# Kernel optimization log

Hardware: AMD Instinct MI355X
Metric: run time of the kernel (lower is better)

Reference implementation:

```python
import jax, jax.numpy as jnp
import numpy as np

H_DIM, W_DIM, D_MODEL = 128, 128, 1024
N_HEADS, HEAD_DIM = 16, 64


def setup_inputs() -> dict:
    key = jax.random.key(0)
    ks = jax.random.split(key, 8)
    s = D_MODEL ** -0.5
    return {
        "hidden_state": jax.random.normal(ks[0], (H_DIM, W_DIM, D_MODEL), jnp.float32),
        "attn_mask": jnp.zeros((1, 1, W_DIM, W_DIM), jnp.float32),
        "cos": jax.random.uniform(ks[1], (H_DIM, W_DIM, 1, HEAD_DIM), jnp.float32),
        "sin": jax.random.uniform(ks[2], (H_DIM, W_DIM, 1, HEAD_DIM), jnp.float32),
        "Wq": jax.random.normal(ks[3], (D_MODEL, N_HEADS * HEAD_DIM), jnp.float32) * s,
        "Wk": jax.random.normal(ks[4], (D_MODEL, N_HEADS * HEAD_DIM), jnp.float32) * s,
        "Wv": jax.random.normal(ks[5], (D_MODEL, N_HEADS * HEAD_DIM), jnp.float32) * s,
        "Wo": jax.random.normal(ks[6], (2 * D_MODEL, D_MODEL), jnp.float32) * s,
    }


def _rotate_half(x):
    x1, x2 = jnp.split(x, 2, axis=-1)
    return jnp.concatenate((-x2, x1), axis=-1)


def reference(hidden_state, attn_mask, cos, sin, Wq, Wk, Wv, Wo):
    h, w, d = hidden_state.shape
    Dh = cos.shape[-1]
    nH = d // Dh
    # projections (no bias) + RoPE on q/k
    q = (hidden_state @ Wq).reshape(h, w, nH, Dh)
    k = (hidden_state @ Wk).reshape(h, w, nH, Dh)
    v = (hidden_state @ Wv).reshape(h, w, nH, Dh)
    q = q * cos + _rotate_half(q) * sin
    k = k * cos + _rotate_half(k) * sin
    # NOTE: original divides by sqrt(hidden_size), not sqrt(head_dim)
    scale = jnp.sqrt(jnp.asarray(d, hidden_state.dtype))
    # ---- width attention: (h, w, nH, Dh) -> (h, nH, w, Dh) ----
    qx, kx, vx = (t.transpose(0, 2, 1, 3) for t in (q, k, v))
    sx = jnp.einsum('ahqd,ahkd->ahqk', qx, kx) / scale + attn_mask  # (h, nH, w, w)
    ow = jnp.einsum('ahqk,ahkd->ahqd', jax.nn.softmax(sx, axis=-1), vx)
    w_weights = ow.transpose(0, 2, 1, 3)  # (h, w, nH, Dh)
    # ---- height attention: (h, w, nH, Dh) -> (w, nH, h, Dh) ----
    qy, ky, vy = (t.transpose(1, 2, 0, 3) for t in (q, k, v))
    my = jnp.transpose(attn_mask, (2, 1, 0, 3))
    sy = jnp.einsum('ahqd,ahkd->ahqk', qy, ky) / scale + my  # (w, nH, h, h)
    oh = jnp.einsum('ahqk,ahkd->ahqd', jax.nn.softmax(sy, axis=-1), vy)
    h_weights = oh.transpose(2, 0, 1, 3)  # (h, w, nH, Dh)
    cat = jnp.concatenate([w_weights.reshape(h, w, d), h_weights.reshape(h, w, d)], axis=-1)
    return cat @ Wo
```

## Files before the change

kernel.cpp:

```cpp
#include <hip/hip_runtime.h>

typedef unsigned short u16;
typedef unsigned int   u32;
typedef __bf16 bf16;
typedef bf16  bf16x8 __attribute__((ext_vector_type(8)));
typedef float f32x4  __attribute__((ext_vector_type(4)));

__device__ __forceinline__ u16 bf16u(float f) {
    u32 x = __builtin_bit_cast(u32, f);
    x += 0x7fffu + ((x >> 16) & 1u);
    return (u16)(x >> 16);
}

__device__ __forceinline__ void gl_lds16(const void* g, void* l) {
    __builtin_amdgcn_global_load_lds(
        (const __attribute__((address_space(1))) u32*)g,
        (__attribute__((address_space(3))) u32*)l, 16, 0, 0);
}

__global__ __launch_bounds__(256) void cvt_x_kernel(const float4* __restrict__ in,
                                                    ushort4* __restrict__ out, int n4) {
    int i = blockIdx.x * 256 + threadIdx.x;
    if (i >= n4) return;
    float4 f = in[i];
    ushort4 o;
    o.x = bf16u(f.x); o.y = bf16u(f.y); o.z = bf16u(f.z); o.w = bf16u(f.w);
    out[i] = o;
}

__global__ __launch_bounds__(256) void transp_all(
    const float* __restrict__ Wq, const float* __restrict__ Wk,
    const float* __restrict__ Wv, const float* __restrict__ Wo,
    u16* __restrict__ WqkvT, u16* __restrict__ WoT)
{
    const int z = blockIdx.z;
    const float* W; u16* WT; int rows, cols;
    if (z < 3) {
        if (blockIdx.y >= 32) return;
        W = (z == 0) ? Wq : (z == 1) ? Wk : Wv;
        WT = WqkvT + (size_t)z * 1024 * 1024;
        rows = 1024; cols = 1024;
    } else {
        W = Wo; WT = WoT; rows = 2048; cols = 1024;
    }
    __shared__ float t[32][33];
    int bx = blockIdx.x * 32, by = blockIdx.y * 32;
    int x = threadIdx.x & 31, y = threadIdx.x >> 5;
#pragma unroll
    for (int i = 0; i < 32; i += 8)
        t[y + i][x] = W[(size_t)(by + y + i) * cols + bx + x];
    __syncthreads();
#pragma unroll
    for (int i = 0; i < 32; i += 8)
        WT[(size_t)(bx + y + i) * rows + by + x] = bf16u(t[x][y + i]);
}

#define BAR   __builtin_amdgcn_s_barrier()
#define SB0   __builtin_amdgcn_sched_barrier(0)
#define VM4   asm volatile("s_waitcnt vmcnt(4)" ::: "memory")
#define VM0   asm volatile("s_waitcnt vmcnt(0)" ::: "memory")

__global__ __launch_bounds__(512, 2) void gemm8(
    const u16* __restrict__ A, const u16* __restrict__ BT, void* __restrict__ Cout,
    const float* __restrict__ cosp, const float* __restrict__ sinp,
    int M, int N, int K, int mode)
{
    __shared__ u16 Ld[3][16384];
    const int tid = threadIdx.x;
    const int wid = tid >> 6, lane = tid & 63;
    const int nx = gridDim.x;
    const int nwg = nx * gridDim.y;
    const int orig = blockIdx.y * nx + blockIdx.x;
    const int vid = (orig & 7) * (nwg >> 3) + (orig >> 3);
    const int m0 = (vid / nx) << 8, n0 = (vid % nx) << 8;
    const int wr = wid >> 2, wc = wid & 3;

    const int srow = tid >> 2;
    const int sl = (tid & 3) ^ ((srow >> 1) & 3);
    const u16* aS0 = A + (size_t)(m0 + srow) * K + (sl << 3);
    const u16* aS1 = aS0 + (size_t)128 * K;
    const u16* bS0 = BT + (size_t)(n0 + srow) * K + (sl << 3);
    const u16* bS1 = bS0 + (size_t)128 * K;
    const int wdb = wid << 9;
    const int nt = K >> 5;

#define STAGE(T, B_) do { if ((T) < nt) { size_t _ko = (size_t)(T) << 5; \
        gl_lds16(aS0 + _ko, &Ld[B_][wdb]); \
        gl_lds16(aS1 + _ko, &Ld[B_][4096 + wdb]); \
        gl_lds16(bS0 + _ko, &Ld[B_][8192 + wdb]); \
        gl_lds16(bS1 + _ko, &Ld[B_][12288 + wdb]); } } while (0)

    const int phys = ((lane >> 4) ^ ((lane >> 1) & 3)) << 3;
    const int raw = ((wr << 7) + (lane & 15)) << 5;
    const int rbw = (((wc << 6) + (lane & 15)) << 5) + 8192;

    f32x4 acc[8][4] = {};

    STAGE(0, 0); STAGE(1, 1);
    VM4;
    BAR; SB0;

    int b = 0, bs = 2;
    for (int t = 0; t < nt; ++t) {
        const u16* Lb = &Ld[b][0];
        bf16x8 fa[8], fb[4];
#pragma unroll
        for (int mi = 0; mi < 8; mi++)
            fa[mi] = *(const bf16x8*)&Lb[raw + (mi << 9) + phys];
#pragma unroll
        for (int ni = 0; ni < 4; ni++)
            fb[ni] = *(const bf16x8*)&Lb[rbw + (ni << 9) + phys];
        STAGE(t + 2, bs);
        BAR;
        __builtin_amdgcn_s_setprio(1);
#pragma unroll
        for (int mi = 0; mi < 8; mi++)
#pragma unroll
            for (int ni = 0; ni < 4; ni++)
                acc[mi][ni] = __builtin_amdgcn_mfma_f32_16x16x32_bf16(
                    fa[mi], fb[ni], acc[mi][ni], 0, 0, 0);
        __builtin_amdgcn_s_setprio(0);
        if (t + 2 < nt) { VM4; } else { VM0; }
        BAR; SB0;
        b = (b == 2) ? 0 : b + 1;
        bs = (bs == 2) ? 0 : bs + 1;
    }
#undef STAGE

    const int colbase = n0 + (wc << 6) + (lane & 15);
    if (mode == 2) {
        float* C = (float*)Cout;
#pragma unroll
        for (int mi = 0; mi < 8; mi++)
#pragma unroll
            for (int r = 0; r < 4; r++) {
                int m = m0 + (wr << 7) + (mi << 4) + ((lane >> 4) << 2) + r;
                float* row = C + (size_t)m * N + colbase;
#pragma unroll
                for (int ni = 0; ni < 4; ni++) row[ni << 4] = acc[mi][ni][r];
            }
    } else if (n0 < 2048) {
        u16* C = (u16*)Cout;
#pragma unroll
        for (int mi = 0; mi < 8; mi++)
#pragma unroll
            for (int r = 0; r < 4; r++) {
                int m = m0 + (wr << 7) + (mi << 4) + ((lane >> 4) << 2) + r;
                const float* cb = cosp + ((size_t)m << 6);
                const float* sb = sinp + ((size_t)m << 6);
                u16* row = C + (size_t)m * N + colbase;
#pragma unroll
                for (int ni = 0; ni < 4; ni++) {
                    int d = (ni << 4) + (lane & 15);
                    float c = cb[d], s = sb[d];
                    float v0 = acc[mi][ni][r];
                    float vr = acc[mi][ni ^ 2][r];
                    float o = fmaf(v0, c, (ni < 2 ? -vr : vr) * s);
                    row[ni << 4] = bf16u(o);
                }
            }
    } else {
        u16* C = (u16*)Cout;
#pragma unroll
        for (int mi = 0; mi < 8; mi++)
#pragma unroll
            for (int r = 0; r < 4; r++) {
                int m = m0 + (wr << 7) + (mi << 4) + ((lane >> 4) << 2) + r;
                u16* row = C + (size_t)m * N + colbase;
#pragma unroll
                for (int ni = 0; ni < 4; ni++) row[ni << 4] = bf16u(acc[mi][ni][r]);
            }
    }
}

__global__ __launch_bounds__(256) void axial_attn(
    const u16* __restrict__ qkv, const float* __restrict__ mask,
    u16* __restrict__ cat)
{
    __shared__ u16 Kl[128 * 64];
    __shared__ u16 VT[64 * 128];
    __shared__ u16 Pl[128 * 128];
    const int hmode = blockIdx.x >> 11;
    const int o2 = blockIdx.x & 2047;
    const int b = (o2 & 7) * 256 + (o2 >> 3);
    const int a = b >> 4, hd = b & 15;
    const int tid = threadIdx.x, wid = tid >> 6, lane = tid & 63;
    const int tmul = hmode ? 128 : 1;
    const int tadd = hmode ? a : (a << 7);
    const size_t hoff = (size_t)hd << 6;

#pragma unroll
    for (int c = 0; c < 4; c++) {
        int row = (wid << 5) + (c << 3) + (lane >> 3);
        int sc = (lane & 7) ^ (row & 7);
        gl_lds16(qkv + (size_t)(row * tmul + tadd) * 3072 + 1024 + hoff + (sc << 3),
                 &Kl[((wid << 5) + (c << 3)) << 6]);
    }
#pragma unroll
    for (int i = 0; i < 4; i++) {
        int cid = tid + (i << 8);
        int j = cid >> 3;
        int d0 = (cid & 7) << 3;
        uint4 raw = *(const uint4*)(qkv + (size_t)(j * tmul + tadd) * 3072 + 2048 + hoff + d0);
        const u16* e = (const u16*)&raw;
#pragma unroll
        for (int t = 0; t < 8; t++) {
            int d = d0 + t;
            VT[(d << 7) + (((j >> 3) ^ (d & 15)) << 3) + (j & 7)] = e[t];
        }
    }
    bf16x8 aq[2][2];
#pragma unroll
    for (int qt = 0; qt < 2; qt++)
#pragma unroll
        for (int ks = 0; ks < 2; ks++) {
            int row = (wid << 5) + (qt << 4) + (lane & 15);
            aq[qt][ks] = *(const bf16x8*)(qkv + (size_t)(row * tmul + tadd) * 3072 + hoff
                                          + (ks << 5) + ((lane >> 4) << 3));
        }
    __syncthreads();

    f32x4 S[2][8] = {};
#pragma unroll
    for (int kt = 0; kt < 8; kt++) {
        bf16x8 bk[2];
#pragma unroll
        for (int ks = 0; ks < 2; ks++) {
            int row = (kt << 4) + (lane & 15);
            int ch = ((ks << 2) + (lane >> 4)) ^ (row & 7);
            bk[ks] = *(const bf16x8*)&Kl[(row << 6) + (ch << 3)];
        }
#pragma unroll
        for (int qt = 0; qt < 2; qt++) {
            S[qt][kt] = __builtin_amdgcn_mfma_f32_16x16x32_bf16(aq[qt][0], bk[0], S[qt][kt], 0, 0, 0);
            S[qt][kt] = __builtin_amdgcn_mfma_f32_16x16x32_bf16(aq[qt][1], bk[1], S[qt][kt], 0, 0, 0);
        }
    }

    const float scale = 0.03125f;
#pragma unroll
    for (int qt = 0; qt < 2; qt++) {
#pragma unroll
        for (int r = 0; r < 4; r++) {
            int qrow = (wid << 5) + (qt << 4) + ((lane >> 4) << 2) + r;
            const float* mrow = mask + (hmode ? (a << 7) : (qrow << 7));
            float mx = -1e30f;
#pragma unroll
            for (int kt = 0; kt < 8; kt++) {
                float sv = fmaf(S[qt][kt][r], scale, mrow[(kt << 4) + (lane & 15)]);
                S[qt][kt][r] = sv;
                mx = fmaxf(mx, sv);
            }
            mx = fmaxf(mx, __shfl_xor(mx, 1));
            mx = fmaxf(mx, __shfl_xor(mx, 2));
            mx = fmaxf(mx, __shfl_xor(mx, 4));
            mx = fmaxf(mx, __shfl_xor(mx, 8));
            float sum = 0.f;
#pragma unroll
            for (int kt = 0; kt < 8; kt++) {
                float p = __expf(S[qt][kt][r] - mx);
                S[qt][kt][r] = p;
                sum += p;
            }
            sum += __shfl_xor(sum, 1);
            sum += __shfl_xor(sum, 2);
            sum += __shfl_xor(sum, 4);
            sum += __shfl_xor(sum, 8);
            float rinv = 1.0f / sum;
#pragma unroll
            for (int kt = 0; kt < 8; kt++) {
                int kcol = (kt << 4) + (lane & 15);
                int ch = (kcol >> 3) ^ (qrow & 15);
                Pl[(qrow << 7) + (ch << 3) + (kcol & 7)] = bf16u(S[qt][kt][r] * rinv);
            }
        }
    }
    __syncthreads();

    f32x4 O[4][2] = {};
#pragma unroll
    for (int ks = 0; ks < 4; ks++) {
        bf16x8 av[4], bp[2];
#pragma unroll
        for (int dt = 0; dt < 4; dt++) {
            int drow = (dt << 4) + (lane & 15);
            int ch = ((ks << 2) + (lane >> 4)) ^ (drow & 15);
            av[dt] = *(const bf16x8*)&VT[(drow << 7) + (ch << 3)];
        }
#pragma unroll
        for (int qt = 0; qt < 2; qt++) {
            int qrow = (wid << 5) + (qt << 4) + (lane & 15);
            int ch = ((ks << 2) + (lane >> 4)) ^ (qrow & 15);
            bp[qt] = *(const bf16x8*)&Pl[(qrow << 7) + (ch << 3)];
        }
#pragma unroll
        for (int dt = 0; dt < 4; dt++)
#pragma unroll
            for (int qt = 0; qt < 2; qt++)
                O[dt][qt] = __builtin_amdgcn_mfma_f32_16x16x32_bf16(av[dt], bp[qt], O[dt][qt], 0, 0, 0);
    }

    const int cbase = (hmode ? 1024 : 0) + (hd << 6);
#pragma unroll
    for (int dt = 0; dt < 4; dt++)
#pragma unroll
        for (int qt = 0; qt < 2; qt++) {
            int qrow = (wid << 5) + (qt << 4) + (lane & 15);
            int d0 = (dt << 4) + ((lane >> 4) << 2);
            size_t base = ((size_t)(qrow * tmul + tadd) << 11) + cbase + d0;
            ushort4 pk;
            pk.x = bf16u(O[dt][qt][0]);
            pk.y = bf16u(O[dt][qt][1]);
            pk.z = bf16u(O[dt][qt][2]);
            pk.w = bf16u(O[dt][qt][3]);
            *(ushort4*)(cat + base) = pk;
        }
}

extern "C" void kernel_launch(void* const* d_in, const int* in_sizes, int n_in,
                              void* d_out, int out_size, void* d_ws, size_t ws_size,
                              hipStream_t stream)
{
    (void)in_sizes; (void)n_in; (void)out_size; (void)ws_size;
    const float* hidden = (const float*)d_in[0];
    const float* mask   = (const float*)d_in[1];
    const float* cosp   = (const float*)d_in[2];
    const float* sinp   = (const float*)d_in[3];
    const float* Wq     = (const float*)d_in[4];
    const float* Wk     = (const float*)d_in[5];
    const float* Wv     = (const float*)d_in[6];
    const float* Wo     = (const float*)d_in[7];

    char* ws = (char*)d_ws;
    u16* Xb    = (u16*)(ws);
    u16* WqkvT = (u16*)(ws + 33554432);
    u16* cat   = (u16*)(ws);
    u16* WoT   = (u16*)(ws + 67108864);
    u16* qkvb  = (u16*)(ws + 71303168);

    cvt_x_kernel<<<16384, 256, 0, stream>>>((const float4*)hidden, (ushort4*)Xb, 4194304);
    transp_all<<<dim3(32, 64, 4), 256, 0, stream>>>(Wq, Wk, Wv, Wo, WqkvT, WoT);

    gemm8<<<dim3(12, 64), 512, 0, stream>>>(Xb, WqkvT, qkvb, cosp, sinp, 16384, 3072, 1024, 1);

    axial_attn<<<4096, 256, 0, stream>>>(qkvb, mask, cat);

    gemm8<<<dim3(4, 64), 512, 0, stream>>>(cat, WoT, d_out, nullptr, nullptr, 16384, 1024, 2048, 2);
}
```

Baseline: 316.9 us.

## Replace triple-buffered 256x256 GEMM with simple single-buffer 128x128 tile GEMM

Swaps the 512-thread, 256x256-tile GEMM with a three-stage LDS pipeline for a 256-thread, 128x128-tile kernel that uses a single LDS buffer. Each K-step loads, then synchronizes, then computes. Grids are doubled in both dimensions to cover the outputs. This reduces LDS and register footprint per block and raises block count, but it drops the load/compute overlap and halves data reuse per tile, which likely exposes memory latency.

```diff
diff --git a/kernel.cpp b/kernel.cpp
--- a/kernel.cpp
+++ b/kernel.cpp
@@ -55,86 +55,69 @@
         WT[(size_t)(bx + y + i) * rows + by + x] = bf16u(t[x][y + i]);
 }
 
-#define BAR   __builtin_amdgcn_s_barrier()
-#define SB0   __builtin_amdgcn_sched_barrier(0)
-#define VM4   asm volatile("s_waitcnt vmcnt(4)" ::: "memory")
-#define VM0   asm volatile("s_waitcnt vmcnt(0)" ::: "memory")
-
-__global__ __launch_bounds__(512, 2) void gemm8(
+__global__ __launch_bounds__(256) void gemm97(
     const u16* __restrict__ A, const u16* __restrict__ BT, void* __restrict__ Cout,
     const float* __restrict__ cosp, const float* __restrict__ sinp,
     int M, int N, int K, int mode)
 {
-    __shared__ u16 Ld[3][16384];
+    __shared__ u16 Ld[8192];
     const int tid = threadIdx.x;
     const int wid = tid >> 6, lane = tid & 63;
     const int nx = gridDim.x;
     const int nwg = nx * gridDim.y;
     const int orig = blockIdx.y * nx + blockIdx.x;
     const int vid = (orig & 7) * (nwg >> 3) + (orig >> 3);
-    const int m0 = (vid / nx) << 8, n0 = (vid % nx) << 8;
-    const int wr = wid >> 2, wc = wid & 3;
+    const int m0 = (vid / nx) << 7, n0 = (vid % nx) << 7;
+    const int wr = wid >> 1, wc = wid & 1;
 
     const int srow = tid >> 2;
-    const int sl = (tid & 3) ^ ((srow >> 1) & 3);
-    const u16* aS0 = A + (size_t)(m0 + srow) * K + (sl << 3);
-    const u16* aS1 = aS0 + (size_t)128 * K;
-    const u16* bS0 = BT + (size_t)(n0 + srow) * K + (sl << 3);
-    const u16* bS1 = bS0 + (size_t)128 * K;
+    const int sg = (tid & 3) ^ ((srow >> 1) & 3);
+    const u16* aS = A + (size_t)(m0 + srow) * K + (sg << 3);
+    const u16* bS = BT + (size_t)(n0 + srow) * K + (sg << 3);
+    const size_t h64K = (size_t)64 * K;
     const int wdb = wid << 9;
     const int nt = K >> 5;
 
-#define STAGE(T, B_) do { if ((T) < nt) { size_t _ko = (size_t)(T) << 5; \
-        gl_lds16(aS0 + _ko, &Ld[B_][wdb]); \
-        gl_lds16(aS1 + _ko, &Ld[B_][4096 + wdb]); \
-        gl_lds16(bS0 + _ko, &Ld[B_][8192 + wdb]); \
-        gl_lds16(bS1 + _ko, &Ld[B_][12288 + wdb]); } } while (0)
-
     const int phys = ((lane >> 4) ^ ((lane >> 1) & 3)) << 3;
-    const int raw = ((wr << 7) + (lane & 15)) << 5;
-    const int rbw = (((wc << 6) + (lane & 15)) << 5) + 8192;
-
-    f32x4 acc[8][4] = {};
-
-    STAGE(0, 0); STAGE(1, 1);
-    VM4;
-    BAR; SB0;
-
-    int b = 0, bs = 2;
+    const int raw = ((wr << 6) + (lane & 15)) << 5;
+    const int rbw = (((wc << 6) + (lane & 15)) << 5) + 4096;
+
+    f32x4 acc[4][4] = {};
+
     for (int t = 0; t < nt; ++t) {
-        const u16* Lb = &Ld[b][0];
-        bf16x8 fa[8], fb[4];
-#pragma unroll
-        for (int mi = 0; mi < 8; mi++)
-            fa[mi] = *(const bf16x8*)&Lb[raw + (mi << 9) + phys];
-#pragma unroll
-        for (int ni = 0; ni < 4; ni++)
-            fb[ni] = *(const bf16x8*)&Lb[rbw + (ni << 9) + phys];
-        STAGE(t + 2, bs);
-        BAR;
+        if (t) __syncthreads();
+        const size_t ko = (size_t)t << 5;
+        gl_lds16(aS + ko,        &Ld[wdb]);
+        gl_lds16(aS + ko + h64K, &Ld[2048 + wdb]);
+        gl_lds16(bS + ko,        &Ld[4096 + wdb]);
+        gl_lds16(bS + ko + h64K, &Ld[6144 + wdb]);
+        __syncthreads();
+
+        bf16x8 af[4], bfr[4];
+#pragma unroll
+        for (int i = 0; i < 4; i++)
+            af[i] = *(const bf16x8*)&Ld[raw + (i << 9) + phys];
+#pragma unroll
+        for (int i = 0; i < 4; i++)
+            bfr[i] = *(const bf16x8*)&Ld[rbw + (i << 9) + phys];
         __builtin_amdgcn_s_setprio(1);
 #pragma unroll
-        for (int mi = 0; mi < 8; mi++)
+        for (int mi = 0; mi < 4; mi++)
 #pragma unroll
             for (int ni = 0; ni < 4; ni++)
                 acc[mi][ni] = __builtin_amdgcn_mfma_f32_16x16x32_bf16(
-                    fa[mi], fb[ni], acc[mi][ni], 0, 0, 0);
+                    af[mi], bfr[ni], acc[mi][ni], 0, 0, 0);
         __builtin_amdgcn_s_setprio(0);
-        if (t + 2 < nt) { VM4; } else { VM0; }
-        BAR; SB0;
-        b = (b == 2) ? 0 : b + 1;
-        bs = (bs == 2) ? 0 : bs + 1;
-    }
-#undef STAGE
+    }
 
     const int colbase = n0 + (wc << 6) + (lane & 15);
     if (mode == 2) {
         float* C = (float*)Cout;
 #pragma unroll
-        for (int mi = 0; mi < 8; mi++)
+        for (int mi = 0; mi < 4; mi++)
 #pragma unroll
             for (int r = 0; r < 4; r++) {
-                int m = m0 + (wr << 7) + (mi << 4) + ((lane >> 4) << 2) + r;
+                int m = m0 + (wr << 6) + (mi << 4) + ((lane >> 4) << 2) + r;
                 float* row = C + (size_t)m * N + colbase;
 #pragma unroll
                 for (int ni = 0; ni < 4; ni++) row[ni << 4] = acc[mi][ni][r];
@@ -142,10 +125,10 @@
     } else if (n0 < 2048) {
         u16* C = (u16*)Cout;
 #pragma unroll
-        for (int mi = 0; mi < 8; mi++)
+        for (int mi = 0; mi < 4; mi++)
 #pragma unroll
             for (int r = 0; r < 4; r++) {
-                int m = m0 + (wr << 7) + (mi << 4) + ((lane >> 4) << 2) + r;
+                int m = m0 + (wr << 6) + (mi << 4) + ((lane >> 4) << 2) + r;
                 const float* cb = cosp + ((size_t)m << 6);
                 const float* sb = sinp + ((size_t)m << 6);
                 u16* row = C + (size_t)m * N + colbase;
@@ -162,10 +145,10 @@
     } else {
         u16* C = (u16*)Cout;
 #pragma unroll
-        for (int mi = 0; mi < 8; mi++)
+        for (int mi = 0; mi < 4; mi++)
 #pragma unroll
             for (int r = 0; r < 4; r++) {
-                int m = m0 + (wr << 7) + (mi << 4) + ((lane >> 4) << 2) + r;
+                int m = m0 + (wr << 6) + (mi << 4) + ((lane >> 4) << 2) + r;
                 u16* row = C + (size_t)m * N + colbase;
 #pragma unroll
                 for (int ni = 0; ni < 4; ni++) row[ni << 4] = bf16u(acc[mi][ni][r]);
@@ -341,9 +324,9 @@
     cvt_x_kernel<<<16384, 256, 0, stream>>>((const float4*)hidden, (ushort4*)Xb, 4194304);
     transp_all<<<dim3(32, 64, 4), 256, 0, stream>>>(Wq, Wk, Wv, Wo, WqkvT, WoT);
 
-    gemm8<<<dim3(12, 64), 512, 0, stream>>>(Xb, WqkvT, qkvb, cosp, sinp, 16384, 3072, 1024, 1);
+    gemm97<<<dim3(24, 128), 256, 0, stream>>>(Xb, WqkvT, qkvb, cosp, sinp, 16384, 3072, 1024, 1);
 
     axial_attn<<<4096, 256, 0, stream>>>(qkvb, mask, cat);
 
-    gemm8<<<dim3(4, 64), 512, 0, stream>>>(cat, WoT, d_out, nullptr, nullptr, 16384, 1024, 2048, 2);
-}
+    gemm97<<<dim3(8, 128), 256, 0, stream>>>(cat, WoT, d_out, nullptr, nullptr, 16384, 1024, 2048, 2);
+}
```

Result: slower. 348.6 us (+10.0%).
